# Optimization experiments

Measured on AMD Instinct MI355X. Metric: run time of the kernel, lower is better.

## Reference

```python
import jax, jax.numpy as jnp
import numpy as np
from jax.ops import segment_sum

N_NODES = 50000
N_EDGES = 800000

def setup_inputs() -> dict:
    key = jax.random.key(0)
    ks = jax.random.split(key, 8)
    def glorot(k, shape):
        fan_in, fan_out = shape
        lim = jnp.sqrt(6.0 / (fan_in + fan_out))
        return jax.random.uniform(k, shape, jnp.float32, -lim, lim)
    return {
        'features': jax.random.normal(ks[0], (N_NODES, 1433), jnp.float32),
        'edge_index': jax.random.randint(ks[1], (2, N_EDGES), 0, N_NODES, jnp.int64),
        'W1': glorot(ks[2], (1433, 256)), 'b1': jnp.zeros((256,), jnp.float32),
        'W2': glorot(ks[3], (256, 32)),  'b2': jnp.zeros((32,), jnp.float32),
        'W3': glorot(ks[4], (32, 7)),    'b3': jnp.zeros((7,), jnp.float32),
    }

def _graph_conv(x, W, b, src, dst, c_src, c_dst, n):
    # DGL GraphConv, norm='both', in_feats > out_feats: weight first, then SpMM.
    h = (x * c_src[:, None]) @ W          # [N, out]
    agg = segment_sum(h[src], dst, num_segments=n)  # sparse neighbor sum
    return agg * c_dst[:, None] + b

def reference(features, edge_index, W1, b1, W2, b2, W3, b3):
    n = features.shape[0]
    src, dst = edge_index[0], edge_index[1]
    ones = jnp.ones((src.shape[0],), jnp.float32)
    deg_out = jnp.maximum(segment_sum(ones, src, num_segments=n), 1.0)
    deg_in = jnp.maximum(segment_sum(ones, dst, num_segments=n), 1.0)
    c_src = jax.lax.rsqrt(deg_out)
    c_dst = jax.lax.rsqrt(deg_in)
    x1 = jax.nn.relu(_graph_conv(features, W1, b1, src, dst, c_src, c_dst, n))
    x2 = jax.nn.relu(_graph_conv(x1, W2, b2, src, dst, c_src, c_dst, n))
    x3 = _graph_conv(x2, W3, b3, src, dst, c_src, c_dst, n)
    return jax.nn.log_softmax(x3, axis=1)
```

## Files before the change

### kernel.cpp

```cpp
#include <hip/hip_runtime.h>
#include <math.h>

typedef unsigned short u16;
typedef unsigned int u32;
typedef __attribute__((ext_vector_type(8))) short bf16x8;
typedef __attribute__((ext_vector_type(4))) float f32x4;

#define NN 50000
#define NE 800000
#define F0 1433
#define KP 1440
#define MP 50048
#define D1 256
#define D2 32
#define NB 196

__device__ __forceinline__ float bf2f(u16 h) { return __uint_as_float(((u32)h) << 16); }
__device__ __forceinline__ u16 f2bf(float f) {
  u32 u = __float_as_uint(f);
  u32 r = (u + 0x7FFFu + ((u >> 16) & 1u)) >> 16;
  return (u16)r;
}

__device__ __forceinline__ void gl16(const void* g, void* l) {
  __builtin_amdgcn_global_load_lds((const __attribute__((address_space(1))) u32*)g,
                                   (__attribute__((address_space(3))) u32*)l, 16, 0, 0);
}

__global__ __launch_bounds__(256) void k_hist(const int* __restrict__ ei,
                                              int* __restrict__ cs, int* __restrict__ cd) {
  const int e = blockIdx.x * 256 + threadIdx.x;
  if (e < NE) {
    atomicAdd(&cs[ei[e]], 1);
    atomicAdd(&cd[ei[NE + e]], 1);
  }
}

__global__ __launch_bounds__(256) void k_scan1(const int* __restrict__ cd, int* __restrict__ bsum) {
  __shared__ int sh[256];
  const int t = threadIdx.x;
  const int i = blockIdx.x * 256 + t;
  sh[t] = (i < NN) ? cd[i] : 0;
  __syncthreads();
  for (int o = 128; o > 0; o >>= 1) {
    if (t < o) sh[t] += sh[t + o];
    __syncthreads();
  }
  if (t == 0) bsum[blockIdx.x] = sh[0];
}

__global__ __launch_bounds__(256) void k_scan2(const int* __restrict__ bsum, int* __restrict__ boff) {
  __shared__ int sh[256];
  const int t = threadIdx.x;
  const int v = (t < NB) ? bsum[t] : 0;
  sh[t] = v;
  __syncthreads();
  for (int o = 1; o < 256; o <<= 1) {
    int x = (t >= o) ? sh[t - o] : 0;
    __syncthreads();
    sh[t] += x;
    __syncthreads();
  }
  if (t < NB) boff[t] = sh[t] - v;
}

__global__ __launch_bounds__(256) void k_scan3(const int* __restrict__ cd, const int* __restrict__ cs,
                                               const int* __restrict__ boff,
                                               int* __restrict__ row, int* __restrict__ cur,
                                               float* __restrict__ cdst, float* __restrict__ csrc) {
  __shared__ int sh[256];
  const int t = threadIdx.x;
  const int i = blockIdx.x * 256 + t;
  const int v = (i < NN) ? cd[i] : 0;
  sh[t] = v;
  __syncthreads();
  for (int o = 1; o < 256; o <<= 1) {
    int x = (t >= o) ? sh[t - o] : 0;
    __syncthreads();
    sh[t] += x;
    __syncthreads();
  }
  if (i < NN) {
    const int start = boff[blockIdx.x] + sh[t] - v;
    row[i] = start;
    cur[i] = start;
    if (i == NN - 1) row[NN] = start + v;
    cdst[i] = rsqrtf(fmaxf((float)v, 1.0f));
    csrc[i] = rsqrtf(fmaxf((float)cs[i], 1.0f));
  }
}

__global__ __launch_bounds__(256) void k_scatter(const int* __restrict__ ei,
                                                 int* __restrict__ cur, int* __restrict__ csr) {
  const int e = blockIdx.x * 256 + threadIdx.x;
  if (e < NE) {
    const int d = ei[NE + e];
    const int p = atomicAdd(&cur[d], 1);
    csr[p] = ei[e];
  }
}

__global__ __launch_bounds__(256) void k_padA(const float* __restrict__ F, u16* __restrict__ P) {
  const int t = blockIdx.x * 256 + threadIdx.x;
  if (t >= 720) return;
  const int i = blockIdx.y;
  const int k = t * 2;
  u32 v = 0;
  if (i < NN) {
    const size_t base = (size_t)i * F0;
    u32 lo = (k < F0) ? (u32)f2bf(F[base + k]) : 0u;
    u32 hi = (k + 1 < F0) ? (u32)f2bf(F[base + k + 1]) : 0u;
    v = lo | (hi << 16);
  }
  *(u32*)(P + (size_t)i * KP + k) = v;
}

__global__ __launch_bounds__(256) void k_prepw(const float* __restrict__ W1, const float* __restrict__ W2,
                                               u16* __restrict__ W1T, u16* __restrict__ W2T) {
  const int b = blockIdx.x, t = threadIdx.x;
  if (b < KP) {
    W1T[(size_t)t * KP + b] = (b < F0) ? f2bf(W1[(size_t)b * D1 + t]) : (u16)0;
  } else {
    const int idx = (b - KP) * 256 + t;
    const int k = idx & 255, n = idx >> 8;
    W2T[n * 256 + k] = f2bf(W2[k * 32 + n]);
  }
}

__global__ __launch_bounds__(256) void k_gemm1(const u16* __restrict__ A, const u16* __restrict__ BT,
                                               const float* __restrict__ csrc, u16* __restrict__ H) {
  __shared__ u16 As[128 * 32];
  __shared__ u16 Bs[128 * 32];
  const int tid = threadIdx.x;
  const int wave = tid >> 6, lane = tid & 63;
  const int l16 = lane & 15, quad = lane >> 4;
  const int waveM = wave & 1, waveN = wave >> 1;
  const int tn = blockIdx.x, tm = blockIdx.y;

  f32x4 acc[4][4];
#pragma unroll
  for (int mi = 0; mi < 4; ++mi)
#pragma unroll
    for (int ni = 0; ni < 4; ++ni) acc[mi][ni] = f32x4{0.f, 0.f, 0.f, 0.f};

  const int c0 = wave * 64 + lane;
  const int rA0 = c0 >> 2, qA0 = (c0 & 3) * 8;
  const u16* Ab = A + (size_t)tm * 128 * KP;
  const u16* Bb = BT + (size_t)tn * 128 * KP;
  u16* As0 = As + (wave * 64) * 8;
  u16* As1 = As + (wave * 64 + 256) * 8;
  u16* Bs0 = Bs + (wave * 64) * 8;
  u16* Bs1 = Bs + (wave * 64 + 256) * 8;
  const size_t off0 = (size_t)rA0 * KP + qA0;
  const size_t off1 = (size_t)(rA0 + 64) * KP + qA0;

  for (int kt = 0; kt < KP / 32; ++kt) {
    const int k0 = kt * 32;
    __syncthreads();
    gl16(Ab + off0 + k0, As0);
    gl16(Ab + off1 + k0, As1);
    gl16(Bb + off0 + k0, Bs0);
    gl16(Bb + off1 + k0, Bs1);
    __syncthreads();
    bf16x8 af[4], bfr[4];
#pragma unroll
    for (int mi = 0; mi < 4; ++mi)
      af[mi] = *(const bf16x8*)(As + ((waveM * 64 + mi * 16 + l16) * 32 + quad * 8));
#pragma unroll
    for (int ni = 0; ni < 4; ++ni)
      bfr[ni] = *(const bf16x8*)(Bs + ((waveN * 64 + ni * 16 + l16) * 32 + quad * 8));
#pragma unroll
    for (int mi = 0; mi < 4; ++mi)
#pragma unroll
      for (int ni = 0; ni < 4; ++ni)
        acc[mi][ni] = __builtin_amdgcn_mfma_f32_16x16x32_bf16(af[mi], bfr[ni], acc[mi][ni], 0, 0, 0);
  }

  const int rbase = tm * 128 + waveM * 64 + quad * 4;
  const int cbase = tn * 128 + waveN * 64 + l16;
#pragma unroll
  for (int mi = 0; mi < 4; ++mi) {
#pragma unroll
    for (int e = 0; e < 4; ++e) {
      const int i = rbase + mi * 16 + e;
      if (i < NN) {
        const float cs = csrc[i];
#pragma unroll
        for (int ni = 0; ni < 4; ++ni)
          H[(size_t)i * D1 + cbase + ni * 16] = f2bf(acc[mi][ni][e] * cs);
      }
    }
  }
}

__global__ __launch_bounds__(256) void k_spmm1f(const int* __restrict__ row, const int* __restrict__ csr,
                                                const u16* __restrict__ h1, const float* __restrict__ cdst,
                                                const float* __restrict__ csrc, const float* __restrict__ b1,
                                                u16* __restrict__ x) {
  const int d = blockIdx.x * 4 + (threadIdx.x >> 6);
  const int lane = threadIdx.x & 63;
  const int rs = row[d], re = row[d + 1];
  float a0 = 0.f, a1 = 0.f, a2 = 0.f, a3 = 0.f;
  int e = rs;
  for (; e + 1 < re; e += 2) {
    const int s0 = csr[e], s1 = csr[e + 1];
    const ushort4 v0 = *(const ushort4*)(h1 + (size_t)s0 * D1 + lane * 4);
    const ushort4 v1 = *(const ushort4*)(h1 + (size_t)s1 * D1 + lane * 4);
    a0 += bf2f(v0.x) + bf2f(v1.x);
    a1 += bf2f(v0.y) + bf2f(v1.y);
    a2 += bf2f(v0.z) + bf2f(v1.z);
    a3 += bf2f(v0.w) + bf2f(v1.w);
  }
  if (e < re) {
    const int s0 = csr[e];
    const ushort4 v0 = *(const ushort4*)(h1 + (size_t)s0 * D1 + lane * 4);
    a0 += bf2f(v0.x); a1 += bf2f(v0.y); a2 += bf2f(v0.z); a3 += bf2f(v0.w);
  }
  const float cd = cdst[d], cs = csrc[d];
  const float4 bb = *(const float4*)(b1 + lane * 4);
  const float r0 = fmaxf(a0 * cd + bb.x, 0.f) * cs;
  const float r1 = fmaxf(a1 * cd + bb.y, 0.f) * cs;
  const float r2 = fmaxf(a2 * cd + bb.z, 0.f) * cs;
  const float r3 = fmaxf(a3 * cd + bb.w, 0.f) * cs;
  ushort4 o;
  o.x = f2bf(r0); o.y = f2bf(r1); o.z = f2bf(r2); o.w = f2bf(r3);
  *(ushort4*)(x + (size_t)d * D1 + lane * 4) = o;
}

__global__ __launch_bounds__(256) void k_gemm2(const u16* __restrict__ A, const u16* __restrict__ BT,
                                               u16* __restrict__ H) {
  __shared__ u16 As[128 * 32];
  __shared__ u16 Bs[32 * 32];
  const int tid = threadIdx.x;
  const int wave = tid >> 6, lane = tid & 63;
  const int l16 = lane & 15, quad = lane >> 4;
  const int tm = blockIdx.x;

  f32x4 acc[2][2];
#pragma unroll
  for (int mi = 0; mi < 2; ++mi)
#pragma unroll
    for (int ni = 0; ni < 2; ++ni) acc[mi][ni] = f32x4{0.f, 0.f, 0.f, 0.f};

  const int r0 = tid >> 2, q0 = (tid & 3) * 8;
  int rowA0 = tm * 128 + r0;      if (rowA0 >= NN) rowA0 = NN - 1;
  int rowA1 = tm * 128 + r0 + 64; if (rowA1 >= NN) rowA1 = NN - 1;
  for (int kt = 0; kt < 8; ++kt) {
    const int k0 = kt * 32;
    __syncthreads();
    uint4 v0 = *(const uint4*)(A + (size_t)rowA0 * D1 + k0 + q0);
    uint4 v1 = *(const uint4*)(A + (size_t)rowA1 * D1 + k0 + q0);
    *(uint4*)(As + r0 * 32 + q0) = v0;
    *(uint4*)(As + (r0 + 64) * 32 + q0) = v1;
    if (tid < 128) {
      uint4 vb = *(const uint4*)(BT + (size_t)r0 * D1 + k0 + q0);
      *(uint4*)(Bs + r0 * 32 + q0) = vb;
    }
    __syncthreads();
    bf16x8 af[2], bfr[2];
#pragma unroll
    for (int mi = 0; mi < 2; ++mi)
      af[mi] = *(const bf16x8*)(As + ((wave * 32 + mi * 16 + l16) * 32 + quad * 8));
#pragma unroll
    for (int ni = 0; ni < 2; ++ni)
      bfr[ni] = *(const bf16x8*)(Bs + ((ni * 16 + l16) * 32 + quad * 8));
#pragma unroll
    for (int mi = 0; mi < 2; ++mi)
#pragma unroll
      for (int ni = 0; ni < 2; ++ni)
        acc[mi][ni] = __builtin_amdgcn_mfma_f32_16x16x32_bf16(af[mi], bfr[ni], acc[mi][ni], 0, 0, 0);
  }

  const int rbase = tm * 128 + wave * 32 + quad * 4;
#pragma unroll
  for (int mi = 0; mi < 2; ++mi)
#pragma unroll
    for (int e = 0; e < 4; ++e) {
      const int i = rbase + mi * 16 + e;
      if (i < NN) {
#pragma unroll
        for (int ni = 0; ni < 2; ++ni)
          H[(size_t)i * D2 + ni * 16 + l16] = f2bf(acc[mi][ni][e]);
      }
    }
}

__global__ __launch_bounds__(256) void k_spmm2f(const int* __restrict__ row, const int* __restrict__ csr,
                                                const u16* __restrict__ h2, const float* __restrict__ cdst,
                                                const float* __restrict__ csrc, const float* __restrict__ b2,
                                                u16* __restrict__ x) {
  const int t = threadIdx.x;
  const int d = blockIdx.x * 8 + (t >> 5);
  const int f = t & 31;
  const int rs = row[d], re = row[d + 1];
  float acc = 0.f;
  int e = rs;
  for (; e + 1 < re; e += 2) {
    const int s0 = csr[e], s1 = csr[e + 1];
    acc += bf2f(h2[(size_t)s0 * D2 + f]) + bf2f(h2[(size_t)s1 * D2 + f]);
  }
  if (e < re) acc += bf2f(h2[(size_t)csr[e] * D2 + f]);
  const float v = acc * cdst[d] + b2[f];
  x[(size_t)d * D2 + f] = f2bf(fmaxf(v, 0.f) * csrc[d]);
}

__global__ __launch_bounds__(256) void k_l3(const u16* __restrict__ x, const float* __restrict__ W3,
                                            float* __restrict__ h3) {
  __shared__ float w3s[224];
  const int t = threadIdx.x;
  if (t < 224) w3s[t] = W3[t];
  __syncthreads();
  const int i = blockIdx.x * 256 + t;
  if (i >= NN) return;
  const uint4* p = (const uint4*)(x + (size_t)i * D2);
  union { uint4 v[4]; u16 s[32]; } u;
  u.v[0] = p[0]; u.v[1] = p[1]; u.v[2] = p[2]; u.v[3] = p[3];
  float acc[7];
#pragma unroll
  for (int c = 0; c < 7; ++c) acc[c] = 0.f;
#pragma unroll
  for (int k = 0; k < 32; ++k) {
    const float xv = bf2f(u.s[k]);
#pragma unroll
    for (int c = 0; c < 7; ++c) acc[c] += xv * w3s[k * 7 + c];
  }
  float* o = h3 + (size_t)i * 8;
#pragma unroll
  for (int c = 0; c < 7; ++c) o[c] = acc[c];
}

__global__ __launch_bounds__(256) void k_spmm3f(const int* __restrict__ row, const int* __restrict__ csr,
                                                const float* __restrict__ h3, const float* __restrict__ cdst,
                                                const float* __restrict__ b3, float* __restrict__ out) {
  const int t = threadIdx.x;
  const int d = blockIdx.x * 32 + (t >> 3);
  const int c = t & 7;
  if (d >= NN) return;
  const int rs = row[d], re = row[d + 1];
  float acc = 0.f;
  for (int e = rs; e < re; ++e) {
    const int s = csr[e];
    if (c < 7) acc += h3[(size_t)s * 8 + c];
  }
  const float v = (c < 7) ? (acc * cdst[d] + b3[c]) : -INFINITY;
  float m = v;
  m = fmaxf(m, __shfl_xor(m, 1));
  m = fmaxf(m, __shfl_xor(m, 2));
  m = fmaxf(m, __shfl_xor(m, 4));
  float s = (c < 7) ? expf(v - m) : 0.f;
  s += __shfl_xor(s, 1);
  s += __shfl_xor(s, 2);
  s += __shfl_xor(s, 4);
  const float l = logf(s);
  if (c < 7) out[(size_t)d * 7 + c] = v - m - l;
}

static const size_t O_CSRC = 0;
static const size_t O_CDST = 200192;
static const size_t O_ROW  = 400384;
static const size_t O_CUR  = 601088;
static const size_t O_CNTS = 801792;
static const size_t O_CNTD = 1002496;
static const size_t O_BSUM = 1203200;
static const size_t O_BOFF = 1204224;
static const size_t O_CSR  = 1205248;
static const size_t O_W1T  = 4405248;
static const size_t O_W2T  = 5142528;
static const size_t O_H1   = 5158912;
static const size_t O_PADA = 30758912;
static const size_t O_X1S  = O_PADA;
static const size_t O_H2   = O_PADA + 25600000;
static const size_t O_X2S  = O_PADA + 28800000;
static const size_t O_H3   = O_PADA + 32000000;

extern "C" void kernel_launch(void* const* d_in, const int* in_sizes, int n_in,
                              void* d_out, int out_size, void* d_ws, size_t ws_size,
                              hipStream_t stream) {
  const float* feat = (const float*)d_in[0];
  const int* ei     = (const int*)d_in[1];
  const float* W1   = (const float*)d_in[2];
  const float* b1   = (const float*)d_in[3];
  const float* W2   = (const float*)d_in[4];
  const float* b2   = (const float*)d_in[5];
  const float* W3   = (const float*)d_in[6];
  const float* b3   = (const float*)d_in[7];
  float* out = (float*)d_out;

  char* ws = (char*)d_ws;
  float* c_src = (float*)(ws + O_CSRC);
  float* c_dst = (float*)(ws + O_CDST);
  int* row  = (int*)(ws + O_ROW);
  int* cur  = (int*)(ws + O_CUR);
  int* cnts = (int*)(ws + O_CNTS);
  int* cntd = (int*)(ws + O_CNTD);
  int* bsum = (int*)(ws + O_BSUM);
  int* boff = (int*)(ws + O_BOFF);
  int* csr  = (int*)(ws + O_CSR);
  u16* W1T  = (u16*)(ws + O_W1T);
  u16* W2T  = (u16*)(ws + O_W2T);
  u16* h1   = (u16*)(ws + O_H1);
  u16* padA = (u16*)(ws + O_PADA);
  u16* x1s  = (u16*)(ws + O_X1S);
  u16* h2   = (u16*)(ws + O_H2);
  u16* x2s  = (u16*)(ws + O_X2S);
  float* h3 = (float*)(ws + O_H3);

  hipMemsetAsync(cnts, 0, (size_t)NN * 4, stream);
  hipMemsetAsync(cntd, 0, (size_t)NN * 4, stream);
  k_hist<<<(NE + 255) / 256, 256, 0, stream>>>(ei, cnts, cntd);
  k_scan1<<<NB, 256, 0, stream>>>(cntd, bsum);
  k_scan2<<<1, 256, 0, stream>>>(bsum, boff);
  k_scan3<<<NB, 256, 0, stream>>>(cntd, cnts, boff, row, cur, c_dst, c_src);
  k_scatter<<<(NE + 255) / 256, 256, 0, stream>>>(ei, cur, csr);

  k_padA<<<dim3(3, MP), 256, 0, stream>>>(feat, padA);
  k_prepw<<<KP + 32, 256, 0, stream>>>(W1, W2, W1T, W2T);

  k_gemm1<<<dim3(2, MP / 128), 256, 0, stream>>>(padA, W1T, c_src, h1);
  k_spmm1f<<<NN / 4, 256, 0, stream>>>(row, csr, h1, c_dst, c_src, b1, x1s);

  k_gemm2<<<MP / 128, 256, 0, stream>>>(x1s, W2T, h2);
  k_spmm2f<<<NN / 8, 256, 0, stream>>>(row, csr, h2, c_dst, c_src, b2, x2s);

  k_l3<<<(NN + 255) / 256, 256, 0, stream>>>(x2s, W3, h3);
  k_spmm3f<<<(NN + 31) / 32, 256, 0, stream>>>(row, csr, h3, c_dst, b3, out);
}
```

Baseline: 779.3 us.

## Fuse prep kernels, vectorize feature padding, swizzle GEMM1 blocks per XCD, unroll SpMM

Merges the histogram kernel with the feature bf16 padding, and the CSR scatter with the weight transpose, so independent work shares launches. The padding now writes 8 bf16 per thread with 16-byte stores through a grid-stride loop. GEMM1 becomes a 1D grid whose block index is remapped so each XCD handles a contiguous range of tiles, aiming to improve L2 reuse of A rows across the two N tiles. The SpMM gathers are unrolled to keep more loads in flight, at the cost of more registers and a more complex launch layout.

Measured after the change: 769.3 us. Within noise of the previous version (-1.3%).

```diff
diff --git a/kernel.cpp b/kernel.cpp
--- a/kernel.cpp
+++ b/kernel.cpp
@@ -14,6 +14,9 @@
 #define D1 256
 #define D2 32
 #define NB 196
+#define HB 3125
+#define PB 2048
+#define SB 3125
 
 __device__ __forceinline__ float bf2f(u16 h) { return __uint_as_float(((u32)h) << 16); }
 __device__ __forceinline__ u16 f2bf(float f) {
@@ -21,18 +24,43 @@
   u32 r = (u + 0x7FFFu + ((u >> 16) & 1u)) >> 16;
   return (u16)r;
 }
+__device__ __forceinline__ u32 pack2(float lo, float hi) {
+  return (u32)f2bf(lo) | ((u32)f2bf(hi) << 16);
+}
 
 __device__ __forceinline__ void gl16(const void* g, void* l) {
   __builtin_amdgcn_global_load_lds((const __attribute__((address_space(1))) u32*)g,
                                    (__attribute__((address_space(3))) u32*)l, 16, 0, 0);
 }
 
-__global__ __launch_bounds__(256) void k_hist(const int* __restrict__ ei,
-                                              int* __restrict__ cs, int* __restrict__ cd) {
-  const int e = blockIdx.x * 256 + threadIdx.x;
-  if (e < NE) {
-    atomicAdd(&cs[ei[e]], 1);
-    atomicAdd(&cd[ei[NE + e]], 1);
+__global__ __launch_bounds__(256) void k_histpad(const int* __restrict__ ei,
+                                                 int* __restrict__ cs, int* __restrict__ cd,
+                                                 const float* __restrict__ F, u16* __restrict__ P) {
+  if (blockIdx.x < HB) {
+    const int e = blockIdx.x * 256 + threadIdx.x;
+    if (e < NE) {
+      atomicAdd(&cs[ei[e]], 1);
+      atomicAdd(&cd[ei[NE + e]], 1);
+    }
+    return;
+  }
+  const int tid0 = (blockIdx.x - HB) * 256 + threadIdx.x;
+  const int NCH = MP * (KP / 8);
+  for (int c = tid0; c < NCH; c += PB * 256) {
+    const int i = c / (KP / 8);
+    const int k = (c - i * (KP / 8)) * 8;
+    uint4 v = {0u, 0u, 0u, 0u};
+    if (i < NN) {
+      const float* fr = F + (size_t)i * F0 + k;
+      float f[8];
+#pragma unroll
+      for (int j = 0; j < 8; ++j) f[j] = (k + j < F0) ? fr[j] : 0.f;
+      v.x = pack2(f[0], f[1]);
+      v.y = pack2(f[2], f[3]);
+      v.z = pack2(f[4], f[5]);
+      v.w = pack2(f[6], f[7]);
+    }
+    *(uint4*)(P + (size_t)i * KP + k) = v;
   }
 }
 
@@ -90,34 +118,22 @@
   }
 }
 
-__global__ __launch_bounds__(256) void k_scatter(const int* __restrict__ ei,
-                                                 int* __restrict__ cur, int* __restrict__ csr) {
-  const int e = blockIdx.x * 256 + threadIdx.x;
-  if (e < NE) {
-    const int d = ei[NE + e];
-    const int p = atomicAdd(&cur[d], 1);
-    csr[p] = ei[e];
-  }
-}
-
-__global__ __launch_bounds__(256) void k_padA(const float* __restrict__ F, u16* __restrict__ P) {
-  const int t = blockIdx.x * 256 + threadIdx.x;
-  if (t >= 720) return;
-  const int i = blockIdx.y;
-  const int k = t * 2;
-  u32 v = 0;
-  if (i < NN) {
-    const size_t base = (size_t)i * F0;
-    u32 lo = (k < F0) ? (u32)f2bf(F[base + k]) : 0u;
-    u32 hi = (k + 1 < F0) ? (u32)f2bf(F[base + k + 1]) : 0u;
-    v = lo | (hi << 16);
-  }
-  *(u32*)(P + (size_t)i * KP + k) = v;
-}
-
-__global__ __launch_bounds__(256) void k_prepw(const float* __restrict__ W1, const float* __restrict__ W2,
-                                               u16* __restrict__ W1T, u16* __restrict__ W2T) {
-  const int b = blockIdx.x, t = threadIdx.x;
+__global__ __launch_bounds__(256) void k_scatprep(const int* __restrict__ ei,
+                                                  int* __restrict__ cur, int* __restrict__ csr,
+                                                  const float* __restrict__ W1, const float* __restrict__ W2,
+                                                  u16* __restrict__ W1T, u16* __restrict__ W2T) {
+  const int bid = blockIdx.x;
+  const int t = threadIdx.x;
+  if (bid < SB) {
+    const int e = bid * 256 + t;
+    if (e < NE) {
+      const int d = ei[NE + e];
+      const int p = atomicAdd(&cur[d], 1);
+      csr[p] = ei[e];
+    }
+    return;
+  }
+  const int b = bid - SB;
   if (b < KP) {
     W1T[(size_t)t * KP + b] = (b < F0) ? f2bf(W1[(size_t)b * D1 + t]) : (u16)0;
   } else {
@@ -135,7 +151,11 @@
   const int wave = tid >> 6, lane = tid & 63;
   const int l16 = lane & 15, quad = lane >> 4;
   const int waveM = wave & 1, waveN = wave >> 1;
-  const int tn = blockIdx.x, tm = blockIdx.y;
+
+  const int wg = blockIdx.x;
+  const int xcd = wg & 7, idx = wg >> 3;
+  const int swz = (xcd < 6) ? xcd * 98 + idx : 588 + (xcd - 6) * 97 + idx;
+  const int tn = swz & 1, tm = swz >> 1;
 
   f32x4 acc[4][4];
 #pragma unroll
@@ -202,16 +222,18 @@
   const int rs = row[d], re = row[d + 1];
   float a0 = 0.f, a1 = 0.f, a2 = 0.f, a3 = 0.f;
   int e = rs;
-  for (; e + 1 < re; e += 2) {
-    const int s0 = csr[e], s1 = csr[e + 1];
+  for (; e + 3 < re; e += 4) {
+    const int s0 = csr[e], s1 = csr[e + 1], s2 = csr[e + 2], s3 = csr[e + 3];
     const ushort4 v0 = *(const ushort4*)(h1 + (size_t)s0 * D1 + lane * 4);
     const ushort4 v1 = *(const ushort4*)(h1 + (size_t)s1 * D1 + lane * 4);
-    a0 += bf2f(v0.x) + bf2f(v1.x);
-    a1 += bf2f(v0.y) + bf2f(v1.y);
-    a2 += bf2f(v0.z) + bf2f(v1.z);
-    a3 += bf2f(v0.w) + bf2f(v1.w);
-  }
-  if (e < re) {
+    const ushort4 v2 = *(const ushort4*)(h1 + (size_t)s2 * D1 + lane * 4);
+    const ushort4 v3 = *(const ushort4*)(h1 + (size_t)s3 * D1 + lane * 4);
+    a0 += (bf2f(v0.x) + bf2f(v1.x)) + (bf2f(v2.x) + bf2f(v3.x));
+    a1 += (bf2f(v0.y) + bf2f(v1.y)) + (bf2f(v2.y) + bf2f(v3.y));
+    a2 += (bf2f(v0.z) + bf2f(v1.z)) + (bf2f(v2.z) + bf2f(v3.z));
+    a3 += (bf2f(v0.w) + bf2f(v1.w)) + (bf2f(v2.w) + bf2f(v3.w));
+  }
+  for (; e < re; ++e) {
     const int s0 = csr[e];
     const ushort4 v0 = *(const ushort4*)(h1 + (size_t)s0 * D1 + lane * 4);
     a0 += bf2f(v0.x); a1 += bf2f(v0.y); a2 += bf2f(v0.z); a3 += bf2f(v0.w);
@@ -295,11 +317,12 @@
   const int rs = row[d], re = row[d + 1];
   float acc = 0.f;
   int e = rs;
-  for (; e + 1 < re; e += 2) {
-    const int s0 = csr[e], s1 = csr[e + 1];
-    acc += bf2f(h2[(size_t)s0 * D2 + f]) + bf2f(h2[(size_t)s1 * D2 + f]);
-  }
-  if (e < re) acc += bf2f(h2[(size_t)csr[e] * D2 + f]);
+  for (; e + 3 < re; e += 4) {
+    const int s0 = csr[e], s1 = csr[e + 1], s2 = csr[e + 2], s3 = csr[e + 3];
+    acc += (bf2f(h2[(size_t)s0 * D2 + f]) + bf2f(h2[(size_t)s1 * D2 + f])) +
+           (bf2f(h2[(size_t)s2 * D2 + f]) + bf2f(h2[(size_t)s3 * D2 + f]));
+  }
+  for (; e < re; ++e) acc += bf2f(h2[(size_t)csr[e] * D2 + f]);
   const float v = acc * cdst[d] + b2[f];
   x[(size_t)d * D2 + f] = f2bf(fmaxf(v, 0.f) * csrc[d]);
 }
@@ -338,9 +361,11 @@
   if (d >= NN) return;
   const int rs = row[d], re = row[d + 1];
   float acc = 0.f;
-  for (int e = rs; e < re; ++e) {
-    const int s = csr[e];
-    if (c < 7) acc += h3[(size_t)s * 8 + c];
+  if (c < 7) {
+    int e = rs;
+    for (; e + 1 < re; e += 2)
+      acc += h3[(size_t)csr[e] * 8 + c] + h3[(size_t)csr[e + 1] * 8 + c];
+    if (e < re) acc += h3[(size_t)csr[e] * 8 + c];
   }
   const float v = (c < 7) ? (acc * cdst[d] + b3[c]) : -INFINITY;
   float m = v;
@@ -407,16 +432,13 @@
 
   hipMemsetAsync(cnts, 0, (size_t)NN * 4, stream);
   hipMemsetAsync(cntd, 0, (size_t)NN * 4, stream);
-  k_hist<<<(NE + 255) / 256, 256, 0, stream>>>(ei, cnts, cntd);
+  k_histpad<<<HB + PB, 256, 0, stream>>>(ei, cnts, cntd, feat, padA);
   k_scan1<<<NB, 256, 0, stream>>>(cntd, bsum);
   k_scan2<<<1, 256, 0, stream>>>(bsum, boff);
   k_scan3<<<NB, 256, 0, stream>>>(cntd, cnts, boff, row, cur, c_dst, c_src);
-  k_scatter<<<(NE + 255) / 256, 256, 0, stream>>>(ei, cur, csr);
-
-  k_padA<<<dim3(3, MP), 256, 0, stream>>>(feat, padA);
-  k_prepw<<<KP + 32, 256, 0, stream>>>(W1, W2, W1T, W2T);
-
-  k_gemm1<<<dim3(2, MP / 128), 256, 0, stream>>>(padA, W1T, c_src, h1);
+  k_scatprep<<<SB + KP + 32, 256, 0, stream>>>(ei, cur, csr, W1, W2, W1T, W2T);
+
+  k_gemm1<<<782, 256, 0, stream>>>(padA, W1T, c_src, h1);
   k_spmm1f<<<NN / 4, 256, 0, stream>>>(row, csr, h1, c_dst, c_src, b1, x1s);
 
   k_gemm2<<<MP / 128, 256, 0, stream>>>(x1s, W2T, h2);
```
